# Kernel tuning notes

Hardware: AMD Instinct MI355X
Metric: run time of the kernel (lower is better)

## Reference

```python
import jax, jax.numpy as jnp
import numpy as np

B, L, C = 4, 4096, 64

def setup_inputs() -> dict:
    key = jax.random.key(0)
    ks = jax.random.split(key, 7)
    s = 1.0 / np.sqrt(C)
    return {
        "x": jax.random.normal(ks[0], (B, L, C), dtype=jnp.float32),
        "Wq": jax.random.normal(ks[1], (C, C), dtype=jnp.float32) * s,
        "bq": jnp.zeros((C,), dtype=jnp.float32),
        "Wk": jax.random.normal(ks[2], (C, C), dtype=jnp.float32) * s,
        "bk": jnp.zeros((C,), dtype=jnp.float32),
        "Wv": jax.random.normal(ks[3], (C, C), dtype=jnp.float32) * s,
        "bv": jnp.zeros((C,), dtype=jnp.float32),
    }

def reference(x, Wq, bq, Wk, bk, Wv, bv):
    # Conv1D kernel_size=1 == pointwise linear over channels
    Q = jnp.einsum('blc,cf->blf', x, Wq) + bq  # [B, L, F]
    K = jnp.einsum('blc,cf->blf', x, Wk) + bk
    V = jnp.einsum('blc,cf->blf', x, Wv) + bv
    F = Wq.shape[1]
    scores = jnp.einsum('bqf,bkf->bqk', Q, K) / jnp.sqrt(jnp.float32(F))  # [B, Lq, Lk]
    # NOTE: original uses tf.keras.layers.Softmax(axis=1) -> normalize over QUERY axis
    attn = jax.nn.softmax(scores, axis=1)
    out = jnp.einsum('bqk,bkf->bqf', attn, V)
    return out + x
```

## Files before the change

kernel.cpp:

```cpp
#include <hip/hip_runtime.h>
#include <math.h>


#define BB 4
#define LL 4096
#define CC 64
#define C2 0.18033688011112042f

typedef __attribute__((ext_vector_type(8)))  short bf16x8;
typedef __attribute__((ext_vector_type(4)))  float f32x4;
typedef __attribute__((ext_vector_type(16))) float f32x16;
typedef __attribute__((ext_vector_type(4)))  unsigned int u32x4;

#define MFMA16(a, b, c) __builtin_amdgcn_mfma_f32_16x16x32_bf16(a, b, c, 0, 0, 0)
#define MFMA32(a, b, c) __builtin_amdgcn_mfma_f32_32x32x16_bf16(a, b, c, 0, 0, 0)
#define EXP2(x) __builtin_amdgcn_exp2f(x)

#define GLD4(dst, voff, base, imm) \
    asm volatile("global_load_dwordx4 %0, %1, %2 offset:%c3" \
                 : "=v"(dst) : "v"(voff), "s"(base), "i"(imm))
#define WAITVM0() asm volatile("s_waitcnt vmcnt(0)" ::: "memory")
#define SBAR() __builtin_amdgcn_sched_barrier(0)
#define PRIO(n) __builtin_amdgcn_s_setprio(n)

static __device__ __forceinline__ bf16x8 asbf(u32x4 v) {
    union { u32x4 a; bf16x8 b; } u; u.a = v; return u.b;
}
static __device__ __forceinline__ unsigned short f2bf(float f) {
    union { float f; unsigned u; } v; v.f = f;
    unsigned r = v.u + 0x7FFFu + ((v.u >> 16) & 1u);
    return (unsigned short)(r >> 16);
}
static __device__ __forceinline__ float bf2f(unsigned short h) {
    union { unsigned u; float f; } v; v.u = ((unsigned)h) << 16; return v.f;
}
static __device__ __forceinline__ bf16x8 pack8(float4 a, float4 b) {
    bf16x8 r;
    r[0] = (short)f2bf(a.x); r[1] = (short)f2bf(a.y);
    r[2] = (short)f2bf(a.z); r[3] = (short)f2bf(a.w);
    r[4] = (short)f2bf(b.x); r[5] = (short)f2bf(b.y);
    r[6] = (short)f2bf(b.z); r[7] = (short)f2bf(b.w);
    return r;
}
static __device__ __forceinline__ unsigned cvtpk(float lo, float hi) {
    unsigned r;
    asm("v_cvt_pk_bf16_f32 %0, %1, %2" : "=v"(r) : "v"(lo), "v"(hi));
    return r;
}
static __device__ __forceinline__ bf16x8 lds_frag(const unsigned short* p) {
    union { uint2 u[2]; bf16x8 b; } t;
    t.u[0] = *(const uint2*)(p);
    t.u[1] = *(const uint2*)(p + 4);
    return t.b;
}
static __device__ __forceinline__ void lds_put(unsigned short* p, u32x4 v) {
    *(uint2*)(p)     = make_uint2(v[0], v[1]);
    *(uint2*)(p + 4) = make_uint2(v[2], v[3]);
}

__global__ __launch_bounds__(512) void k_qkv(
    const float* __restrict__ x,
    const float* __restrict__ Wq, const float* __restrict__ bq,
    const float* __restrict__ Wk, const float* __restrict__ bk,
    const float* __restrict__ Wv, const float* __restrict__ bv,
    unsigned short* __restrict__ Qb, unsigned short* __restrict__ Kb,
    unsigned short* __restrict__ Vt)
{
    __shared__ float Wl[64 * 64];
    __shared__ unsigned short ldsV[64 * 72];
    const int bid = blockIdx.x;
    const int mat = bid % 3;
    const int r0 = (bid / 3) * 64;
    const int tid = threadIdx.x, w = tid >> 6, lane = tid & 63;
    const int c = lane & 15, g = lane >> 4;
    const int rw = (w >> 1) * 16;
    const int c0 = (w & 1) * 32;

    const float* W  = (mat == 0) ? Wq : (mat == 1) ? Wk : Wv;
    const float* bs = (mat == 0) ? bq : (mat == 1) ? bk : bv;

    {
        const float4* wsrc = (const float4*)W;
        float4* wdst = (float4*)Wl;
        wdst[tid] = wsrc[tid];
        wdst[tid + 512] = wsrc[tid + 512];
    }

    const float* xr = x + (size_t)(r0 + rw + c) * CC;
    const bf16x8 ax0 = pack8(((const float4*)xr)[2 * g], ((const float4*)xr)[2 * g + 1]);
    const bf16x8 ax1 = pack8(((const float4*)xr)[8 + 2 * g], ((const float4*)xr)[8 + 2 * g + 1]);
    __syncthreads();

    f32x4 acc0 = {0.f, 0.f, 0.f, 0.f}, acc1 = {0.f, 0.f, 0.f, 0.f};
    {
        const int col = c0 + c;
        bf16x8 b0, b1;
        #pragma unroll
        for (int j = 0; j < 8; ++j) {
            b0[j] = (short)f2bf(Wl[(8 * g + j) * 64 + col]);
            b1[j] = (short)f2bf(Wl[(32 + 8 * g + j) * 64 + col]);
        }
        acc0 = MFMA16(ax0, b0, acc0); acc0 = MFMA16(ax1, b1, acc0);
    }
    {
        const int col = c0 + 16 + c;
        bf16x8 b0, b1;
        #pragma unroll
        for (int j = 0; j < 8; ++j) {
            b0[j] = (short)f2bf(Wl[(8 * g + j) * 64 + col]);
            b1[j] = (short)f2bf(Wl[(32 + 8 * g + j) * 64 + col]);
        }
        acc1 = MFMA16(ax0, b0, acc1); acc1 = MFMA16(ax1, b1, acc1);
    }
    const float bias0 = bs[c0 + c], bias1 = bs[c0 + 16 + c];

    if (mat < 2) {
        unsigned short* dst = (mat == 0) ? Qb : Kb;
        #pragma unroll
        for (int r = 0; r < 4; ++r) {
            const size_t row = (size_t)(r0 + rw + 4 * g + r) * CC;
            dst[row + c0 + c]      = f2bf(acc0[r] + bias0);
            dst[row + c0 + 16 + c] = f2bf(acc1[r] + bias1);
        }
    } else {
        #pragma unroll
        for (int r = 0; r < 4; ++r) {
            const int rowin = rw + 4 * g + r;
            ldsV[(c0 + c) * 72 + rowin]      = f2bf(acc0[r] + bias0);
            ldsV[(c0 + 16 + c) * 72 + rowin] = f2bf(acc1[r] + bias1);
        }
        __syncthreads();
        const int b = r0 >> 12, ktb = (r0 & 4095) >> 5;
        const int h = tid >> 8, f = (tid >> 2) & 63, ch = tid & 3;
        *(uint4*)(Vt + ((size_t)(b * 128 + ktb + h) * 64 + f) * 32 + ch * 8)
            = *(const uint4*)(ldsV + f * 72 + h * 32 + ch * 8);
    }
}

__global__ __launch_bounds__(512, 4) void k_stats(
    const unsigned short* __restrict__ Qb, const unsigned short* __restrict__ Kb,
    unsigned short* __restrict__ Vt)
{
    const int nb = ((blockIdx.x & 7) << 6) | (blockIdx.x >> 3);
    const int b = nb >> 7, kt32 = nb & 127;
    const int kbase = kt32 * 32;
    const int tid = threadIdx.x, w = tid >> 6, lane = tid & 63;
    const int l31 = lane & 31, hi = lane >> 5;

    __shared__ unsigned short qsm[8][2][32 * 68];
    __shared__ float pl[8][32];
    __shared__ float rls[32];

    const unsigned short* kr = Kb + ((size_t)b * LL + kbase + l31) * CC + 8 * hi;
    const bf16x8 ak0 = *(const bf16x8*)(kr);
    const bf16x8 ak1 = *(const bf16x8*)(kr + 16);
    const bf16x8 ak2 = *(const bf16x8*)(kr + 32);
    const bf16x8 ak3 = *(const bf16x8*)(kr + 48);

    const unsigned short* const sQ = Qb + (size_t)b * LL * CC;
    const unsigned wqoff = (unsigned)(w * 65536);
    const int wb = (lane >> 3) * 68 + (lane & 7) * 8;
    unsigned short* const q0b = &qsm[w][0][0];
    unsigned short* const q1b = &qsm[w][1][0];

    u32x4 S0, S1, S2, S3;
    #define QISS(s_) do { \
        const unsigned vo = wqoff + (unsigned)((s_) * 4096 + lane * 16); \
        GLD4(S0, vo, sQ, 0);    GLD4(S1, vo, sQ, 1024); \
        GLD4(S2, vo, sQ, 2048); GLD4(S3, vo, sQ, 3072); \
    } while (0)
    #define QWR(dst) do { \
        unsigned short* _p = (dst) + wb; \
        lds_put(_p, S0);        lds_put(_p + 544, S1); \
        lds_put(_p + 1088, S2); lds_put(_p + 1632, S3); \
    } while (0)

    QISS(0); WAITVM0(); SBAR(); QWR(q0b); QISS(1);

    f32x16 lacc = {};
    for (int s = 0; s < 16; ++s) {
        const unsigned short* qp = ((s & 1) ? q1b : q0b) + l31 * 68 + hi * 8;
        const bf16x8 b0 = lds_frag(qp);
        const bf16x8 b1 = lds_frag(qp + 16);
        const bf16x8 b2 = lds_frag(qp + 32);
        const bf16x8 b3 = lds_frag(qp + 48);
        f32x16 T = {};
        PRIO(1);
        T = MFMA32(ak0, b0, T); T = MFMA32(ak1, b1, T);
        T = MFMA32(ak2, b2, T); T = MFMA32(ak3, b3, T);
        PRIO(0);
        #pragma unroll
        for (int r = 0; r < 16; ++r) lacc[r] += EXP2(T[r] * C2);
        if (s < 15) {
            WAITVM0(); SBAR();
            QWR((s & 1) ? q0b : q1b);
            if (s < 14) QISS(s + 2);
        }
    }
    #undef QISS
    #undef QWR

    #pragma unroll
    for (int r = 0; r < 16; ++r) {
        float v = lacc[r];
        v += __shfl_xor(v, 1);  v += __shfl_xor(v, 2);
        v += __shfl_xor(v, 4);  v += __shfl_xor(v, 8);
        v += __shfl_xor(v, 16);
        lacc[r] = v;
    }
    if (l31 == 0) {
        #pragma unroll
        for (int r = 0; r < 16; ++r)
            pl[w][(r & 3) + 8 * (r >> 2) + 4 * hi] = lacc[r];
    }
    __syncthreads();
    if (tid < 32) {
        float L = 0.f;
        #pragma unroll
        for (int ww = 0; ww < 8; ++ww) L += pl[ww][tid];
        rls[tid] = 1.0f / L;
    }
    __syncthreads();

    {
        unsigned short* vbase = Vt + ((size_t)(b * 128 + kt32)) * 2048;
        const int kin0 = (tid & 7) * 4;
        ushort4 v = *(const ushort4*)(vbase + tid * 4);
        v.x = f2bf(bf2f(v.x) * rls[kin0 + 0]);
        v.y = f2bf(bf2f(v.y) * rls[kin0 + 1]);
        v.z = f2bf(bf2f(v.z) * rls[kin0 + 2]);
        v.w = f2bf(bf2f(v.w) * rls[kin0 + 3]);
        *(ushort4*)(vbase + tid * 4) = v;
    }
}

__global__ __launch_bounds__(512, 2) void k_out(
    const float* __restrict__ x,
    const unsigned short* __restrict__ Qb, const unsigned short* __restrict__ Kb,
    const unsigned short* __restrict__ Vt,
    float* __restrict__ out)
{
    const int nb = ((blockIdx.x & 7) << 5) | (blockIdx.x >> 3);
    const int b = nb >> 6, qt = nb & 63;
    const int q0 = qt * 64;
    const int tid = threadIdx.x, w = tid >> 6, lane = tid & 63;
    const int l31 = lane & 31, hi = lane >> 5;

    __shared__ unsigned short ksm[8][32 * 68];
    __shared__ unsigned short vsm[8][64 * 36];

    const unsigned short* qrA = Qb + ((size_t)b * LL + q0 + l31) * CC + 8 * hi;
    const unsigned short* qrB = qrA + 32 * CC;
    const bf16x8 qA0 = *(const bf16x8*)(qrA);
    const bf16x8 qA1 = *(const bf16x8*)(qrA + 16);
    const bf16x8 qA2 = *(const bf16x8*)(qrA + 32);
    const bf16x8 qA3 = *(const bf16x8*)(qrA + 48);
    const bf16x8 qB0 = *(const bf16x8*)(qrB);
    const bf16x8 qB1 = *(const bf16x8*)(qrB + 16);
    const bf16x8 qB2 = *(const bf16x8*)(qrB + 32);
    const bf16x8 qB3 = *(const bf16x8*)(qrB + 48);

    const unsigned short* const sK = Kb + (size_t)b * LL * CC;
    const unsigned short* const sV = Vt + (size_t)b * 128 * 2048;
    const unsigned wkoff = (unsigned)(w * 65536);
    const unsigned wvoff = (unsigned)(w * 65536);
    const int kwb = (lane >> 3) * 68 + (lane & 7) * 8;
    const int vwb = (lane >> 2) * 36 + (lane & 3) * 8;

    u32x4 K0, K1, K2, K3, V0, V1, V2, V3;
    #define KISS(s_) do { \
        const unsigned vo = wkoff + (unsigned)((s_) * 4096 + lane * 16); \
        GLD4(K0, vo, sK, 0);    GLD4(K1, vo, sK, 1024); \
        GLD4(K2, vo, sK, 2048); GLD4(K3, vo, sK, 3072); \
    } while (0)
    #define VISS(s_) do { \
        const unsigned vo = wvoff + (unsigned)((s_) * 4096 + lane * 16); \
        GLD4(V0, vo, sV, 0);    GLD4(V1, vo, sV, 1024); \
        GLD4(V2, vo, sV, 2048); GLD4(V3, vo, sV, 3072); \
    } while (0)
    #define KWR() do { \
        unsigned short* _p = &ksm[w][0] + kwb; \
        lds_put(_p, K0);        lds_put(_p + 544, K1); \
        lds_put(_p + 1088, K2); lds_put(_p + 1632, K3); \
    } while (0)
    #define VWR() do { \
        unsigned short* _p = &vsm[w][0] + vwb; \
        lds_put(_p, V0);        lds_put(_p + 576, V1); \
        lds_put(_p + 1152, V2); lds_put(_p + 1728, V3); \
    } while (0)

    KISS(0); VISS(0); WAITVM0(); SBAR();
    KWR(); VWR();
    KISS(1); VISS(1);

    f32x16 oA0 = {}, oA1 = {}, oB0 = {}, oB1 = {};

    for (int s = 0; s < 16; ++s) {
        const unsigned short* kp = &ksm[w][0] + l31 * 68 + hi * 8;
        const bf16x8 a0 = lds_frag(kp);
        const bf16x8 a1 = lds_frag(kp + 16);
        const bf16x8 a2 = lds_frag(kp + 32);
        const bf16x8 a3 = lds_frag(kp + 48);
        f32x16 TA = {}, TB = {};
        PRIO(1);
        TA = MFMA32(a0, qA0, TA); TA = MFMA32(a1, qA1, TA);
        TA = MFMA32(a2, qA2, TA); TA = MFMA32(a3, qA3, TA);
        TB = MFMA32(a0, qB0, TB); TB = MFMA32(a1, qB1, TB);
        TB = MFMA32(a2, qB2, TB); TB = MFMA32(a3, qB3, TB);
        PRIO(0);
        unsigned a0u = cvtpk(EXP2(TA[0] * C2),  EXP2(TA[1] * C2));
        unsigned a1u = cvtpk(EXP2(TA[2] * C2),  EXP2(TA[3] * C2));
        unsigned a2u = cvtpk(EXP2(TA[4] * C2),  EXP2(TA[5] * C2));
        unsigned a3u = cvtpk(EXP2(TA[6] * C2),  EXP2(TA[7] * C2));
        unsigned a4u = cvtpk(EXP2(TA[8] * C2),  EXP2(TA[9] * C2));
        unsigned a5u = cvtpk(EXP2(TA[10] * C2), EXP2(TA[11] * C2));
        unsigned a6u = cvtpk(EXP2(TA[12] * C2), EXP2(TA[13] * C2));
        unsigned a7u = cvtpk(EXP2(TA[14] * C2), EXP2(TA[15] * C2));
        unsigned b0u = cvtpk(EXP2(TB[0] * C2),  EXP2(TB[1] * C2));
        unsigned b1u = cvtpk(EXP2(TB[2] * C2),  EXP2(TB[3] * C2));
        unsigned b2u = cvtpk(EXP2(TB[4] * C2),  EXP2(TB[5] * C2));
        unsigned b3u = cvtpk(EXP2(TB[6] * C2),  EXP2(TB[7] * C2));
        unsigned b4u = cvtpk(EXP2(TB[8] * C2),  EXP2(TB[9] * C2));
        unsigned b5u = cvtpk(EXP2(TB[10] * C2), EXP2(TB[11] * C2));
        unsigned b6u = cvtpk(EXP2(TB[12] * C2), EXP2(TB[13] * C2));
        unsigned b7u = cvtpk(EXP2(TB[14] * C2), EXP2(TB[15] * C2));
        asm volatile("s_nop 1");
        asm("v_permlane32_swap_b32 %0, %1" : "+v"(a0u), "+v"(a2u));
        asm("v_permlane32_swap_b32 %0, %1" : "+v"(a1u), "+v"(a3u));
        asm("v_permlane32_swap_b32 %0, %1" : "+v"(a4u), "+v"(a6u));
        asm("v_permlane32_swap_b32 %0, %1" : "+v"(a5u), "+v"(a7u));
        asm("v_permlane32_swap_b32 %0, %1" : "+v"(b0u), "+v"(b2u));
        asm("v_permlane32_swap_b32 %0, %1" : "+v"(b1u), "+v"(b3u));
        asm("v_permlane32_swap_b32 %0, %1" : "+v"(b4u), "+v"(b6u));
        asm("v_permlane32_swap_b32 %0, %1" : "+v"(b5u), "+v"(b7u));
        u32x4 fA1, fA2, fB1, fB2;
        fA1[0] = a0u; fA1[1] = a1u; fA1[2] = a2u; fA1[3] = a3u;
        fA2[0] = a4u; fA2[1] = a5u; fA2[2] = a6u; fA2[3] = a7u;
        fB1[0] = b0u; fB1[1] = b1u; fB1[2] = b2u; fB1[3] = b3u;
        fB2[0] = b4u; fB2[1] = b5u; fB2[2] = b6u; fB2[3] = b7u;
        const unsigned short* vp0 = &vsm[w][0] + l31 * 36 + hi * 8;
        const unsigned short* vp1 = &vsm[w][0] + (32 + l31) * 36 + hi * 8;
        const bf16x8 v00 = lds_frag(vp0);
        const bf16x8 v01 = lds_frag(vp0 + 16);
        const bf16x8 v10 = lds_frag(vp1);
        const bf16x8 v11 = lds_frag(vp1 + 16);
        PRIO(1);
        oA0 = MFMA32(v00, asbf(fA1), oA0);
        oA0 = MFMA32(v01, asbf(fA2), oA0);
        oA1 = MFMA32(v10, asbf(fA1), oA1);
        oA1 = MFMA32(v11, asbf(fA2), oA1);
        oB0 = MFMA32(v00, asbf(fB1), oB0);
        oB0 = MFMA32(v01, asbf(fB2), oB0);
        oB1 = MFMA32(v10, asbf(fB1), oB1);
        oB1 = MFMA32(v11, asbf(fB2), oB1);
        PRIO(0);
        if (s < 15) {
            WAITVM0(); SBAR();
            KWR(); VWR();
            if (s < 14) { KISS(s + 2); VISS(s + 2); }
        }
    }
    #undef KISS
    #undef VISS
    #undef KWR
    #undef VWR

    __syncthreads();
    float* ocomb = (float*)&ksm[0][0];
    for (int i = tid; i < 64 * 68; i += 512) ocomb[i] = 0.f;
    __syncthreads();
    #pragma unroll
    for (int r = 0; r < 16; ++r) {
        const int fr = (r & 3) + 8 * (r >> 2) + 4 * hi;
        atomicAdd(&ocomb[l31 * 68 + fr],             oA0[r]);
        atomicAdd(&ocomb[l31 * 68 + 32 + fr],        oA1[r]);
        atomicAdd(&ocomb[(32 + l31) * 68 + fr],      oB0[r]);
        atomicAdd(&ocomb[(32 + l31) * 68 + 32 + fr], oB1[r]);
    }
    __syncthreads();
    {
        const int q = tid >> 3, f8 = (tid & 7) * 8;
        const size_t row = (size_t)b * LL + q0 + q;
        const float4 xv0 = ((const float4*)(x + row * CC))[f8 >> 2];
        const float4 xv1 = ((const float4*)(x + row * CC))[(f8 >> 2) + 1];
        const float4 ov0 = *(const float4*)(&ocomb[q * 68 + f8]);
        const float4 ov1 = *(const float4*)(&ocomb[q * 68 + f8 + 4]);
        ((float4*)(out + row * CC))[f8 >> 2] =
            make_float4(xv0.x + ov0.x, xv0.y + ov0.y, xv0.z + ov0.z, xv0.w + ov0.w);
        ((float4*)(out + row * CC))[(f8 >> 2) + 1] =
            make_float4(xv1.x + ov1.x, xv1.y + ov1.y, xv1.z + ov1.z, xv1.w + ov1.w);
    }
}

extern "C" void kernel_launch(void* const* d_in, const int* in_sizes, int n_in,
                              void* d_out, int out_size, void* d_ws, size_t ws_size,
                              hipStream_t stream)
{
    const float* x  = (const float*)d_in[0];
    const float* Wq = (const float*)d_in[1];
    const float* bq = (const float*)d_in[2];
    const float* Wk = (const float*)d_in[3];
    const float* bk = (const float*)d_in[4];
    const float* Wv = (const float*)d_in[5];
    const float* bv = (const float*)d_in[6];
    float* out = (float*)d_out;

    const size_t n = (size_t)BB * LL * CC;
    unsigned short* Qb = (unsigned short*)d_ws;
    unsigned short* Kb = Qb + n;
    unsigned short* Vt = Kb + n;

    hipLaunchKernelGGL(k_qkv, dim3(3 * BB * LL / 64), dim3(512), 0, stream,
                       x, Wq, bq, Wk, bk, Wv, bv, Qb, Kb, Vt);
    hipLaunchKernelGGL(k_stats, dim3(BB * (LL / 32)), dim3(512), 0, stream,
                       Qb, Kb, Vt);
    hipLaunchKernelGGL(k_out, dim3(BB * (LL / 64)), dim3(512), 0, stream,
                       x, Qb, Kb, Vt, out);
}
```

Before: 97.07 us.

## Store Q/K/V in MFMA fragment layout and stream tiles via global_load_lds

The QKV kernel now writes Q, K and V already arranged in MFMA fragment order, tile by tile. The stats and output kernels use direct global-to-LDS loads with a double buffer and vmcnt-based waits, so tiles no longer pass through registers into padded LDS. The stats kernel now handles 64 keys per block with two accumulators, which halves the grid, and the launch bound is relaxed to 2. Priority hints are removed. The risks are bank conflicts in the unpadded LDS layout and lower occupancy.

```diff
diff --git a/kernel.cpp b/kernel.cpp
--- a/kernel.cpp
+++ b/kernel.cpp
@@ -16,12 +16,14 @@
 #define MFMA32(a, b, c) __builtin_amdgcn_mfma_f32_32x32x16_bf16(a, b, c, 0, 0, 0)
 #define EXP2(x) __builtin_amdgcn_exp2f(x)
 
-#define GLD4(dst, voff, base, imm) \
-    asm volatile("global_load_dwordx4 %0, %1, %2 offset:%c3" \
-                 : "=v"(dst) : "v"(voff), "s"(base), "i"(imm))
+#define GLDS(gp, lp) __builtin_amdgcn_global_load_lds( \
+    (const __attribute__((address_space(1))) unsigned int*)(gp), \
+    (__attribute__((address_space(3))) unsigned int*)(lp), 16, 0, 0)
 #define WAITVM0() asm volatile("s_waitcnt vmcnt(0)" ::: "memory")
+#define WAITVM4() asm volatile("s_waitcnt vmcnt(4)" ::: "memory")
+#define WAITVM8() asm volatile("s_waitcnt vmcnt(8)" ::: "memory")
+#define LGKM0()   asm volatile("s_waitcnt lgkmcnt(0)" ::: "memory")
 #define SBAR() __builtin_amdgcn_sched_barrier(0)
-#define PRIO(n) __builtin_amdgcn_s_setprio(n)
 
 static __device__ __forceinline__ bf16x8 asbf(u32x4 v) {
     union { u32x4 a; bf16x8 b; } u; u.a = v; return u.b;
@@ -47,16 +49,7 @@
     asm("v_cvt_pk_bf16_f32 %0, %1, %2" : "=v"(r) : "v"(lo), "v"(hi));
     return r;
 }
-static __device__ __forceinline__ bf16x8 lds_frag(const unsigned short* p) {
-    union { uint2 u[2]; bf16x8 b; } t;
-    t.u[0] = *(const uint2*)(p);
-    t.u[1] = *(const uint2*)(p + 4);
-    return t.b;
-}
-static __device__ __forceinline__ void lds_put(unsigned short* p, u32x4 v) {
-    *(uint2*)(p)     = make_uint2(v[0], v[1]);
-    *(uint2*)(p + 4) = make_uint2(v[2], v[3]);
-}
+
 
 __global__ __launch_bounds__(512) void k_qkv(
     const float* __restrict__ x,
@@ -68,6 +61,7 @@
 {
     __shared__ float Wl[64 * 64];
     __shared__ unsigned short ldsV[64 * 72];
+    __shared__ unsigned short ldsF[4096];
     const int bid = blockIdx.x;
     const int mat = bid % 3;
     const int r0 = (bid / 3) * 64;
@@ -115,13 +109,21 @@
     const float bias0 = bs[c0 + c], bias1 = bs[c0 + 16 + c];
 
     if (mat < 2) {
+        #pragma unroll
+        for (int r = 0; r < 4; ++r) {
+            const int row = rw + 4 * g + r;
+            const int tl = row >> 5, lr = row & 31;
+            const int col0 = c0 + c;
+            ldsF[tl * 2048 + (col0 >> 4) * 512 + (((col0 >> 3) & 1) * 32 + lr) * 8 + (col0 & 7)]
+                = f2bf(acc0[r] + bias0);
+            const int col1 = c0 + 16 + c;
+            ldsF[tl * 2048 + (col1 >> 4) * 512 + (((col1 >> 3) & 1) * 32 + lr) * 8 + (col1 & 7)]
+                = f2bf(acc1[r] + bias1);
+        }
+        __syncthreads();
         unsigned short* dst = (mat == 0) ? Qb : Kb;
-        #pragma unroll
-        for (int r = 0; r < 4; ++r) {
-            const size_t row = (size_t)(r0 + rw + 4 * g + r) * CC;
-            dst[row + c0 + c]      = f2bf(acc0[r] + bias0);
-            dst[row + c0 + 16 + c] = f2bf(acc1[r] + bias1);
-        }
+        *(uint4*)(dst + ((size_t)(r0 >> 5)) * 2048 + tid * 8) =
+            *(const uint4*)(ldsF + tid * 8);
     } else {
         #pragma unroll
         for (int r = 0; r < 4; ++r) {
@@ -131,90 +133,96 @@
         }
         __syncthreads();
         const int b = r0 >> 12, ktb = (r0 & 4095) >> 5;
-        const int h = tid >> 8, f = (tid >> 2) & 63, ch = tid & 3;
-        *(uint4*)(Vt + ((size_t)(b * 128 + ktb + h) * 64 + f) * 32 + ch * 8)
-            = *(const uint4*)(ldsV + f * 72 + h * 32 + ch * 8);
-    }
-}
-
-__global__ __launch_bounds__(512, 4) void k_stats(
+        const int f = tid >> 3, ch = tid & 7;
+        const size_t dtile = (size_t)(b * 128 + ktb + (ch >> 2));
+        const size_t didx = dtile * 2048
+            + (size_t)(((f >> 5) * 2 + ((ch >> 1) & 1)) * 512
+                       + ((ch & 1) * 32 + (f & 31)) * 8);
+        *(uint4*)(Vt + didx) = *(const uint4*)(ldsV + f * 72 + ch * 8);
+    }
+}
+
+__global__ __launch_bounds__(512, 2) void k_stats(
     const unsigned short* __restrict__ Qb, const unsigned short* __restrict__ Kb,
     unsigned short* __restrict__ Vt)
 {
-    const int nb = ((blockIdx.x & 7) << 6) | (blockIdx.x >> 3);
-    const int b = nb >> 7, kt32 = nb & 127;
-    const int kbase = kt32 * 32;
+    const int nb = ((blockIdx.x & 7) << 5) | (blockIdx.x >> 3);
+    const int b = nb >> 6, kt = nb & 63;
     const int tid = threadIdx.x, w = tid >> 6, lane = tid & 63;
     const int l31 = lane & 31, hi = lane >> 5;
-
-    __shared__ unsigned short qsm[8][2][32 * 68];
-    __shared__ float pl[8][32];
-    __shared__ float rls[32];
-
-    const unsigned short* kr = Kb + ((size_t)b * LL + kbase + l31) * CC + 8 * hi;
-    const bf16x8 ak0 = *(const bf16x8*)(kr);
-    const bf16x8 ak1 = *(const bf16x8*)(kr + 16);
-    const bf16x8 ak2 = *(const bf16x8*)(kr + 32);
-    const bf16x8 ak3 = *(const bf16x8*)(kr + 48);
-
-    const unsigned short* const sQ = Qb + (size_t)b * LL * CC;
-    const unsigned wqoff = (unsigned)(w * 65536);
-    const int wb = (lane >> 3) * 68 + (lane & 7) * 8;
-    unsigned short* const q0b = &qsm[w][0][0];
-    unsigned short* const q1b = &qsm[w][1][0];
-
-    u32x4 S0, S1, S2, S3;
-    #define QISS(s_) do { \
-        const unsigned vo = wqoff + (unsigned)((s_) * 4096 + lane * 16); \
-        GLD4(S0, vo, sQ, 0);    GLD4(S1, vo, sQ, 1024); \
-        GLD4(S2, vo, sQ, 2048); GLD4(S3, vo, sQ, 3072); \
+    const int w_u = __builtin_amdgcn_readfirstlane(w);
+
+    __shared__ unsigned short qsm[8][2][2048];
+    __shared__ float pl[8][64];
+    __shared__ float rls[64];
+
+    const char* Kt = (const char*)Kb + ((size_t)(b * 128 + kt * 2)) * 4096 + lane * 16;
+    const bf16x8 akA0 = *(const bf16x8*)(Kt);
+    const bf16x8 akA1 = *(const bf16x8*)(Kt + 1024);
+    const bf16x8 akA2 = *(const bf16x8*)(Kt + 2048);
+    const bf16x8 akA3 = *(const bf16x8*)(Kt + 3072);
+    const bf16x8 akB0 = *(const bf16x8*)(Kt + 4096);
+    const bf16x8 akB1 = *(const bf16x8*)(Kt + 5120);
+    const bf16x8 akB2 = *(const bf16x8*)(Kt + 6144);
+    const bf16x8 akB3 = *(const bf16x8*)(Kt + 7168);
+
+    const char* const gQ = (const char*)Qb + ((size_t)(b * 128 + w * 16)) * 4096 + lane * 16;
+
+    #define QISS(s_, buf_) do { \
+        const char* _g = gQ + (size_t)(s_) * 4096; \
+        char* _l = (char*)&qsm[w_u][buf_][0]; \
+        GLDS(_g, _l);              GLDS(_g + 1024, _l + 1024); \
+        GLDS(_g + 2048, _l + 2048); GLDS(_g + 3072, _l + 3072); \
     } while (0)
-    #define QWR(dst) do { \
-        unsigned short* _p = (dst) + wb; \
-        lds_put(_p, S0);        lds_put(_p + 544, S1); \
-        lds_put(_p + 1088, S2); lds_put(_p + 1632, S3); \
-    } while (0)
-
-    QISS(0); WAITVM0(); SBAR(); QWR(q0b); QISS(1);
-
-    f32x16 lacc = {};
+
+    QISS(0, 0); QISS(1, 1);
+
+    f32x16 laccA = {}, laccB = {};
+    #pragma unroll 2
     for (int s = 0; s < 16; ++s) {
-        const unsigned short* qp = ((s & 1) ? q1b : q0b) + l31 * 68 + hi * 8;
-        const bf16x8 b0 = lds_frag(qp);
-        const bf16x8 b1 = lds_frag(qp + 16);
-        const bf16x8 b2 = lds_frag(qp + 32);
-        const bf16x8 b3 = lds_frag(qp + 48);
-        f32x16 T = {};
-        PRIO(1);
-        T = MFMA32(ak0, b0, T); T = MFMA32(ak1, b1, T);
-        T = MFMA32(ak2, b2, T); T = MFMA32(ak3, b3, T);
-        PRIO(0);
-        #pragma unroll
-        for (int r = 0; r < 16; ++r) lacc[r] += EXP2(T[r] * C2);
-        if (s < 15) {
-            WAITVM0(); SBAR();
-            QWR((s & 1) ? q0b : q1b);
-            if (s < 14) QISS(s + 2);
+        const int buf = s & 1;
+        if (s < 15) { WAITVM4(); } else { WAITVM0(); }
+        SBAR();
+        const char* qp = (const char*)&qsm[w_u][buf][0] + lane * 16;
+        const bf16x8 q0 = *(const bf16x8*)(qp);
+        const bf16x8 q1 = *(const bf16x8*)(qp + 1024);
+        const bf16x8 q2 = *(const bf16x8*)(qp + 2048);
+        const bf16x8 q3 = *(const bf16x8*)(qp + 3072);
+        LGKM0(); SBAR();
+        if (s < 14) QISS(s + 2, buf);
+        f32x16 TA = {}, TB = {};
+        TA = MFMA32(akA0, q0, TA); TA = MFMA32(akA1, q1, TA);
+        TA = MFMA32(akA2, q2, TA); TA = MFMA32(akA3, q3, TA);
+        TB = MFMA32(akB0, q0, TB); TB = MFMA32(akB1, q1, TB);
+        TB = MFMA32(akB2, q2, TB); TB = MFMA32(akB3, q3, TB);
+        #pragma unroll
+        for (int r = 0; r < 16; ++r) {
+            laccA[r] += EXP2(TA[r] * C2);
+            laccB[r] += EXP2(TB[r] * C2);
         }
     }
     #undef QISS
-    #undef QWR
 
     #pragma unroll
     for (int r = 0; r < 16; ++r) {
-        float v = lacc[r];
-        v += __shfl_xor(v, 1);  v += __shfl_xor(v, 2);
-        v += __shfl_xor(v, 4);  v += __shfl_xor(v, 8);
-        v += __shfl_xor(v, 16);
-        lacc[r] = v;
+        float va = laccA[r], vb = laccB[r];
+        va += __shfl_xor(va, 1);  vb += __shfl_xor(vb, 1);
+        va += __shfl_xor(va, 2);  vb += __shfl_xor(vb, 2);
+        va += __shfl_xor(va, 4);  vb += __shfl_xor(vb, 4);
+        va += __shfl_xor(va, 8);  vb += __shfl_xor(vb, 8);
+        va += __shfl_xor(va, 16); vb += __shfl_xor(vb, 16);
+        laccA[r] = va; laccB[r] = vb;
     }
     if (l31 == 0) {
         #pragma unroll
-        for (int r = 0; r < 16; ++r)
-            pl[w][(r & 3) + 8 * (r >> 2) + 4 * hi] = lacc[r];
-    }
-    __syncthreads();
-    if (tid < 32) {
+        for (int r = 0; r < 16; ++r) {
+            const int kr = (r & 3) + 8 * (r >> 2) + 4 * hi;
+            pl[w][kr]      = laccA[r];
+            pl[w][32 + kr] = laccB[r];
+        }
+    }
+    __syncthreads();
+    if (tid < 64) {
         float L = 0.f;
         #pragma unroll
         for (int ww = 0; ww < 8; ++ww) L += pl[ww][tid];
@@ -222,15 +230,17 @@
     }
     __syncthreads();
 
-    {
-        unsigned short* vbase = Vt + ((size_t)(b * 128 + kt32)) * 2048;
-        const int kin0 = (tid & 7) * 4;
-        ushort4 v = *(const ushort4*)(vbase + tid * 4);
-        v.x = f2bf(bf2f(v.x) * rls[kin0 + 0]);
-        v.y = f2bf(bf2f(v.y) * rls[kin0 + 1]);
-        v.z = f2bf(bf2f(v.z) * rls[kin0 + 2]);
-        v.w = f2bf(bf2f(v.w) * rls[kin0 + 3]);
-        *(ushort4*)(vbase + tid * 4) = v;
+    #pragma unroll
+    for (int i = 0; i < 2; ++i) {
+        unsigned short* base = Vt + ((size_t)(b * 128 + kt * 2 + i)) * 2048;
+        const int frag = tid >> 7, lane16 = (tid & 127) >> 1, j0 = (tid & 1) * 4;
+        const int kin = (frag & 1) * 16 + (lane16 >> 5) * 8 + j0;
+        ushort4 v = *(const ushort4*)(base + tid * 4);
+        v.x = f2bf(bf2f(v.x) * rls[i * 32 + kin + 0]);
+        v.y = f2bf(bf2f(v.y) * rls[i * 32 + kin + 1]);
+        v.z = f2bf(bf2f(v.z) * rls[i * 32 + kin + 2]);
+        v.w = f2bf(bf2f(v.w) * rls[i * 32 + kin + 3]);
+        *(ushort4*)(base + tid * 4) = v;
     }
 }
 
@@ -245,69 +255,61 @@
     const int q0 = qt * 64;
     const int tid = threadIdx.x, w = tid >> 6, lane = tid & 63;
     const int l31 = lane & 31, hi = lane >> 5;
-
-    __shared__ unsigned short ksm[8][32 * 68];
-    __shared__ unsigned short vsm[8][64 * 36];
-
-    const unsigned short* qrA = Qb + ((size_t)b * LL + q0 + l31) * CC + 8 * hi;
-    const unsigned short* qrB = qrA + 32 * CC;
-    const bf16x8 qA0 = *(const bf16x8*)(qrA);
-    const bf16x8 qA1 = *(const bf16x8*)(qrA + 16);
-    const bf16x8 qA2 = *(const bf16x8*)(qrA + 32);
-    const bf16x8 qA3 = *(const bf16x8*)(qrA + 48);
-    const bf16x8 qB0 = *(const bf16x8*)(qrB);
-    const bf16x8 qB1 = *(const bf16x8*)(qrB + 16);
-    const bf16x8 qB2 = *(const bf16x8*)(qrB + 32);
-    const bf16x8 qB3 = *(const bf16x8*)(qrB + 48);
-
-    const unsigned short* const sK = Kb + (size_t)b * LL * CC;
-    const unsigned short* const sV = Vt + (size_t)b * 128 * 2048;
-    const unsigned wkoff = (unsigned)(w * 65536);
-    const unsigned wvoff = (unsigned)(w * 65536);
-    const int kwb = (lane >> 3) * 68 + (lane & 7) * 8;
-    const int vwb = (lane >> 2) * 36 + (lane & 3) * 8;
-
-    u32x4 K0, K1, K2, K3, V0, V1, V2, V3;
-    #define KISS(s_) do { \
-        const unsigned vo = wkoff + (unsigned)((s_) * 4096 + lane * 16); \
-        GLD4(K0, vo, sK, 0);    GLD4(K1, vo, sK, 1024); \
-        GLD4(K2, vo, sK, 2048); GLD4(K3, vo, sK, 3072); \
+    const int w_u = __builtin_amdgcn_readfirstlane(w);
+
+    __shared__ unsigned short ksm[8][2][2048];
+    __shared__ unsigned short vsm[8][2][2048];
+
+    const char* Qt0 = (const char*)Qb + ((size_t)(b * 128 + qt * 2)) * 4096 + lane * 16;
+    const bf16x8 qA0 = *(const bf16x8*)(Qt0);
+    const bf16x8 qA1 = *(const bf16x8*)(Qt0 + 1024);
+    const bf16x8 qA2 = *(const bf16x8*)(Qt0 + 2048);
+    const bf16x8 qA3 = *(const bf16x8*)(Qt0 + 3072);
+    const bf16x8 qB0 = *(const bf16x8*)(Qt0 + 4096);
+    const bf16x8 qB1 = *(const bf16x8*)(Qt0 + 5120);
+    const bf16x8 qB2 = *(const bf16x8*)(Qt0 + 6144);
+    const bf16x8 qB3 = *(const bf16x8*)(Qt0 + 7168);
+
+    const char* const gK = (const char*)Kb + ((size_t)(b * 128 + w * 16)) * 4096 + lane * 16;
+    const char* const gV = (const char*)Vt + ((size_t)(b * 128 + w * 16)) * 4096 + lane * 16;
+
+    #define ISS(s_, buf_) do { \
+        const char* _gk = gK + (size_t)(s_) * 4096; \
+        const char* _gv = gV + (size_t)(s_) * 4096; \
+        char* _lk = (char*)&ksm[w_u][buf_][0]; \
+        char* _lv = (char*)&vsm[w_u][buf_][0]; \
+        GLDS(_gk, _lk);              GLDS(_gk + 1024, _lk + 1024); \
+        GLDS(_gk + 2048, _lk + 2048); GLDS(_gk + 3072, _lk + 3072); \
+        GLDS(_gv, _lv);              GLDS(_gv + 1024, _lv + 1024); \
+        GLDS(_gv + 2048, _lv + 2048); GLDS(_gv + 3072, _lv + 3072); \
     } while (0)
-    #define VISS(s_) do { \
-        const unsigned vo = wvoff + (unsigned)((s_) * 4096 + lane * 16); \
-        GLD4(V0, vo, sV, 0);    GLD4(V1, vo, sV, 1024); \
-        GLD4(V2, vo, sV, 2048); GLD4(V3, vo, sV, 3072); \
-    } while (0)
-    #define KWR() do { \
-        unsigned short* _p = &ksm[w][0] + kwb; \
-        lds_put(_p, K0);        lds_put(_p + 544, K1); \
-        lds_put(_p + 1088, K2); lds_put(_p + 1632, K3); \
-    } while (0)
-    #define VWR() do { \
-        unsigned short* _p = &vsm[w][0] + vwb; \
-        lds_put(_p, V0);        lds_put(_p + 576, V1); \
-        lds_put(_p + 1152, V2); lds_put(_p + 1728, V3); \
-    } while (0)
-
-    KISS(0); VISS(0); WAITVM0(); SBAR();
-    KWR(); VWR();
-    KISS(1); VISS(1);
+
+    ISS(0, 0); ISS(1, 1);
 
     f32x16 oA0 = {}, oA1 = {}, oB0 = {}, oB1 = {};
 
+    #pragma unroll 2
     for (int s = 0; s < 16; ++s) {
-        const unsigned short* kp = &ksm[w][0] + l31 * 68 + hi * 8;
-        const bf16x8 a0 = lds_frag(kp);
-        const bf16x8 a1 = lds_frag(kp + 16);
-        const bf16x8 a2 = lds_frag(kp + 32);
-        const bf16x8 a3 = lds_frag(kp + 48);
+        const int buf = s & 1;
+        if (s < 15) { WAITVM8(); } else { WAITVM0(); }
+        SBAR();
+        const char* kp = (const char*)&ksm[w_u][buf][0] + lane * 16;
+        const char* vp = (const char*)&vsm[w_u][buf][0] + lane * 16;
+        const bf16x8 a0  = *(const bf16x8*)(kp);
+        const bf16x8 a1  = *(const bf16x8*)(kp + 1024);
+        const bf16x8 a2  = *(const bf16x8*)(kp + 2048);
+        const bf16x8 a3  = *(const bf16x8*)(kp + 3072);
+        const bf16x8 v00 = *(const bf16x8*)(vp);
+        const bf16x8 v01 = *(const bf16x8*)(vp + 1024);
+        const bf16x8 v10 = *(const bf16x8*)(vp + 2048);
+        const bf16x8 v11 = *(const bf16x8*)(vp + 3072);
+        LGKM0(); SBAR();
+        if (s < 14) ISS(s + 2, buf);
         f32x16 TA = {}, TB = {};
-        PRIO(1);
         TA = MFMA32(a0, qA0, TA); TA = MFMA32(a1, qA1, TA);
         TA = MFMA32(a2, qA2, TA); TA = MFMA32(a3, qA3, TA);
         TB = MFMA32(a0, qB0, TB); TB = MFMA32(a1, qB1, TB);
         TB = MFMA32(a2, qB2, TB); TB = MFMA32(a3, qB3, TB);
-        PRIO(0);
         unsigned a0u = cvtpk(EXP2(TA[0] * C2),  EXP2(TA[1] * C2));
         unsigned a1u = cvtpk(EXP2(TA[2] * C2),  EXP2(TA[3] * C2));
         unsigned a2u = cvtpk(EXP2(TA[4] * C2),  EXP2(TA[5] * C2));
@@ -338,13 +340,6 @@
         fA2[0] = a4u; fA2[1] = a5u; fA2[2] = a6u; fA2[3] = a7u;
         fB1[0] = b0u; fB1[1] = b1u; fB1[2] = b2u; fB1[3] = b3u;
         fB2[0] = b4u; fB2[1] = b5u; fB2[2] = b6u; fB2[3] = b7u;
-        const unsigned short* vp0 = &vsm[w][0] + l31 * 36 + hi * 8;
-        const unsigned short* vp1 = &vsm[w][0] + (32 + l31) * 36 + hi * 8;
-        const bf16x8 v00 = lds_frag(vp0);
-        const bf16x8 v01 = lds_frag(vp0 + 16);
-        const bf16x8 v10 = lds_frag(vp1);
-        const bf16x8 v11 = lds_frag(vp1 + 16);
-        PRIO(1);
         oA0 = MFMA32(v00, asbf(fA1), oA0);
         oA0 = MFMA32(v01, asbf(fA2), oA0);
         oA1 = MFMA32(v10, asbf(fA1), oA1);
@@ -353,20 +348,11 @@
         oB0 = MFMA32(v01, asbf(fB2), oB0);
         oB1 = MFMA32(v10, asbf(fB1), oB1);
         oB1 = MFMA32(v11, asbf(fB2), oB1);
-        PRIO(0);
-        if (s < 15) {
-            WAITVM0(); SBAR();
-            KWR(); VWR();
-            if (s < 14) { KISS(s + 2); VISS(s + 2); }
-        }
-    }
-    #undef KISS
-    #undef VISS
-    #undef KWR
-    #undef VWR
-
-    __syncthreads();
-    float* ocomb = (float*)&ksm[0][0];
+    }
+    #undef ISS
+
+    __syncthreads();
+    float* ocomb = (float*)&ksm[0][0][0];
     for (int i = tid; i < 64 * 68; i += 512) ocomb[i] = 0.f;
     __syncthreads();
     #pragma unroll
@@ -412,7 +398,7 @@
 
     hipLaunchKernelGGL(k_qkv, dim3(3 * BB * LL / 64), dim3(512), 0, stream,
                        x, Wq, bq, Wk, bk, Wv, bv, Qb, Kb, Vt);
-    hipLaunchKernelGGL(k_stats, dim3(BB * (LL / 32)), dim3(512), 0, stream,
+    hipLaunchKernelGGL(k_stats, dim3(BB * (LL / 64)), dim3(512), 0, stream,
                        Qb, Kb, Vt);
     hipLaunchKernelGGL(k_out, dim3(BB * (LL / 64)), dim3(512), 0, stream,
                        x, Qb, Kb, Vt, out);
```

After: 91.66 us. 5.6% less time.
